# Performance work log

Measured on AMD Instinct MI355X. Metric: run time of the kernel, lower is better.

The kernel has to match this reference:

```python
import jax, jax.numpy as jnp
import numpy as np

B, L, HS = 2, 2048, 2048
NH, NKV, HD = 16, 4, 128
EPS = 1e-6
ROPE_BASE = 10000.0
SCALE = HD ** -0.5


def setup_inputs() -> dict:
    key = jax.random.key(0)
    ks = jax.random.split(key, 5)
    w = lambda k, shape: (jax.random.normal(k, shape, jnp.float32) * 0.02)
    return {
        "hidden_states": jax.random.normal(ks[0], (B, L, HS), jnp.float32),
        "Wq": w(ks[1], (HS, NH * HD)),
        "Wk": w(ks[2], (HS, NKV * HD)),
        "Wv": w(ks[3], (HS, NKV * HD)),
        "Wo": w(ks[4], (NH * HD, HS)),
        "q_norm_w": jnp.ones((HD,), jnp.float32),
        "k_norm_w": jnp.ones((HD,), jnp.float32),
    }


def _rmsnorm(x, w):
    return x * jax.lax.rsqrt(jnp.mean(x * x, axis=-1, keepdims=True) + EPS) * w


def _rope(x, cos, sin):
    # x: [B, L, heads, HD]; cos/sin: [1, L, 1, HD//2]
    x1, x2 = jnp.split(x, 2, axis=-1)
    return jnp.concatenate([x1 * cos - x2 * sin, x2 * cos + x1 * sin], axis=-1)


def reference(hidden_states, Wq, Wk, Wv, Wo, q_norm_w, k_norm_w):
    b, l, _ = hidden_states.shape
    n_rep = NH // NKV
    q = (hidden_states @ Wq).reshape(b, l, NH, HD)
    k = (hidden_states @ Wk).reshape(b, l, NKV, HD)
    v = (hidden_states @ Wv).reshape(b, l, NKV, HD)
    # QK RMSNorm over head_dim
    q = _rmsnorm(q, q_norm_w)
    k = _rmsnorm(k, k_norm_w)
    # RoPE with position_ids = arange(L)
    pos = jnp.arange(l, dtype=jnp.float32)
    inv_freq = 1.0 / (ROPE_BASE ** (jnp.arange(0, HD, 2, dtype=jnp.float32) / HD))
    ang = pos[:, None] * inv_freq  # [L, HD//2]
    cos = jnp.cos(ang)[None, :, None, :]
    sin = jnp.sin(ang)[None, :, None, :]
    q = _rope(q, cos, sin)
    k = _rope(k, cos, sin)
    # GQA: torch expand+reshape gives q head h -> kv head (h mod NKV);
    # reshape q to [B, L, n_rep, NKV, HD] (h = r*NKV + j) and contract per kv group.
    qg = q.reshape(b, l, n_rep, NKV, HD)
    scores = jnp.einsum("blrjd,bmjd->brjlm", qg, k) * SCALE  # [B, r, j, L, L]
    causal = jnp.tril(jnp.ones((l, l), dtype=bool))
    scores = jnp.where(causal, scores, -jnp.inf)
    probs = jax.nn.softmax(scores, axis=-1)
    out = jnp.einsum("brjlm,bmjd->blrjd", probs, v).reshape(b, l, NH * HD)
    return out @ Wo
```

## Files before the change

### kernel.cpp

```cpp
#include <hip/hip_runtime.h>
#include <hip/hip_bf16.h>

#define B_  2
#define L_  2048
#define HS_ 2048
#define NH_ 16
#define NKV_ 4
#define HD_ 128
#define EPS_ 1e-6f
#define SCALE_ 0.08838834764831843f
#define LOG2E_ 1.4426950408889634f

typedef __attribute__((ext_vector_type(8))) short bf16x8;
typedef __attribute__((ext_vector_type(4))) float f32x4;

__device__ __forceinline__ f32x4 mfma16(bf16x8 a, bf16x8 b, f32x4 c) {
    return __builtin_amdgcn_mfma_f32_16x16x32_bf16(a, b, c, 0, 0, 0);
}

__device__ __forceinline__ void async_copy16(void* lds, const void* g) {
    __builtin_amdgcn_global_load_lds(
        (const __attribute__((address_space(1))) unsigned int*)g,
        (__attribute__((address_space(3))) unsigned int*)lds,
        16, 0, 0);
}

__device__ __forceinline__ unsigned cvtpk(float lo, float hi) {
    unsigned r;
    asm("v_cvt_pk_bf16_f32 %0, %1, %2" : "=v"(r) : "v"(lo), "v"(hi));
    return r;
}

__global__ __launch_bounds__(256) void cvt_f32_bf16(const float* __restrict__ src,
                                                    __hip_bfloat16* __restrict__ dst,
                                                    int n4) {
    int i = blockIdx.x * 256 + threadIdx.x;
    if (i >= n4) return;
    float4 v = ((const float4*)src)[i];
    union { __hip_bfloat16 h[4]; short4 s; } u;
    u.h[0] = __float2bfloat16(v.x);
    u.h[1] = __float2bfloat16(v.y);
    u.h[2] = __float2bfloat16(v.z);
    u.h[3] = __float2bfloat16(v.w);
    ((short4*)dst)[i] = u.s;
}

__global__ __launch_bounds__(256) void transpose_cvt(const float* __restrict__ src,
                                                     __hip_bfloat16* __restrict__ dst,
                                                     int K, int N) {
    __shared__ float tile[32][33];
    int n0 = blockIdx.x * 32, k0 = blockIdx.y * 32;
    int tx = threadIdx.x & 31, ty = threadIdx.x >> 5;
#pragma unroll
    for (int i = 0; i < 32; i += 8)
        tile[ty + i][tx] = src[(size_t)(k0 + ty + i) * N + n0 + tx];
    __syncthreads();
#pragma unroll
    for (int i = 0; i < 32; i += 8)
        dst[(size_t)(n0 + ty + i) * K + k0 + tx] = __float2bfloat16(tile[tx][ty + i]);
}

__global__ __launch_bounds__(256) void v_transpose(const float* __restrict__ KV,
                                                   __hip_bfloat16* __restrict__ Vt) {
    __shared__ float tile[32][33];
    int bkv = blockIdx.z;
    int b = bkv >> 2, kv = bkv & 3;
    int l0 = blockIdx.x * 32, d0 = blockIdx.y * 32;
    int tx = threadIdx.x & 31, ty = threadIdx.x >> 5;
#pragma unroll
    for (int i = 0; i < 32; i += 8)
        tile[ty + i][tx] = KV[(size_t)(b * L_ + l0 + ty + i) * 1024 + 512 + kv * HD_ + d0 + tx];
    __syncthreads();
#pragma unroll
    for (int i = 0; i < 32; i += 8)
        Vt[((size_t)(b * NKV_ + kv) * HD_ + d0 + ty + i) * L_ + l0 + tx] =
            __float2bfloat16(tile[tx][ty + i]);
}

#define BM 128
#define BN 128
#define BKK 64
__global__ __launch_bounds__(256, 2) void gemm_bf16(const __hip_bfloat16* __restrict__ A,
                                                    const __hip_bfloat16* __restrict__ Bt,
                                                    float* __restrict__ C,
                                                    int M, int N, int K) {
    __shared__ __align__(16) __hip_bfloat16 sA[BM * BKK];
    __shared__ __align__(16) __hip_bfloat16 sB[BN * BKK];
    int t = threadIdx.x;
    int wave = t >> 6, lane = t & 63;
    int row16 = lane & 15, quad = lane >> 4;
    int m0 = blockIdx.x * BM, n0 = blockIdx.y * BN;
    int waveM = (wave >> 1) * 64, waveN = (wave & 1) * 64;
    f32x4 acc[4][4] = {};

    for (int k0 = 0; k0 < K; k0 += BKK) {
#pragma unroll
        for (int i = 0; i < 4; ++i) {
            int c = i * 256 + t;
            int r = c >> 3, kc = (c & 7) * 8;
            async_copy16(&sA[c * 8], A + (size_t)(m0 + r) * K + k0 + kc);
            async_copy16(&sB[c * 8], Bt + (size_t)(n0 + r) * K + k0 + kc);
        }
        __syncthreads();
#pragma unroll
        for (int kc = 0; kc < 2; ++kc) {
            bf16x8 a[4], b[4];
#pragma unroll
            for (int i = 0; i < 4; ++i)
                a[i] = *(const bf16x8*)&sA[(waveM + i * 16 + row16) * BKK + kc * 32 + quad * 8];
#pragma unroll
            for (int j = 0; j < 4; ++j)
                b[j] = *(const bf16x8*)&sB[(waveN + j * 16 + row16) * BKK + kc * 32 + quad * 8];
#pragma unroll
            for (int i = 0; i < 4; ++i)
#pragma unroll
                for (int j = 0; j < 4; ++j)
                    acc[i][j] = mfma16(a[i], b[j], acc[i][j]);
        }
        __syncthreads();
    }
#pragma unroll
    for (int i = 0; i < 4; ++i)
#pragma unroll
        for (int j = 0; j < 4; ++j) {
            int rbase = m0 + waveM + i * 16 + quad * 4;
            int col = n0 + waveN + j * 16 + row16;
#pragma unroll
            for (int r = 0; r < 4; ++r)
                C[(size_t)(rbase + r) * N + col] = acc[i][j][r];
        }
}

__global__ __launch_bounds__(256) void norm_rope(const float* __restrict__ X,
                                                 __hip_bfloat16* __restrict__ Y,
                                                 const float* __restrict__ w,
                                                 int log2nh, int in_stride, float oscale) {
    int row = blockIdx.x * 4 + (threadIdx.x >> 6);
    int lane = threadIdx.x & 63;
    int m = row >> log2nh;
    int head = row & ((1 << log2nh) - 1);
    int pos = m & (L_ - 1);
    const float* x = X + (size_t)m * in_stride + head * HD_;
    float x1 = x[lane], x2 = x[lane + 64];
    float ss = x1 * x1 + x2 * x2;
#pragma unroll
    for (int mm = 1; mm < 64; mm <<= 1) ss += __shfl_xor(ss, mm);
    float rms = rsqrtf(ss * (1.0f / 128.0f) + EPS_);
    float xn1 = x1 * rms * w[lane];
    float xn2 = x2 * rms * w[lane + 64];
    float inv_freq = __builtin_exp2f(-(float)lane * 0.20762050593046014f);
    float ang = (float)pos * inv_freq;
    float c = cosf(ang), s = sinf(ang);
    __hip_bfloat16* y = Y + (size_t)row * HD_;
    y[lane]      = __float2bfloat16((xn1 * c - xn2 * s) * oscale);
    y[lane + 64] = __float2bfloat16((xn2 * c + xn1 * s) * oscale);
}

__global__ __launch_bounds__(256, 2) void flash_attn(const __hip_bfloat16* __restrict__ Q,
                                                     const __hip_bfloat16* __restrict__ Kb,
                                                     const __hip_bfloat16* __restrict__ Vt,
                                                     __hip_bfloat16* __restrict__ O) {
    __shared__ __align__(16) __hip_bfloat16 sK[2][64 * 128];
    __shared__ __align__(16) __hip_bfloat16 sV[2][128 * 64];
    __shared__ __align__(16) __hip_bfloat16 sP[4][16 * 72];

    int t = threadIdx.x, wave = t >> 6, lane = t & 63;
    int row16 = lane & 15, quad = lane >> 4;
    int h = blockIdx.y, b = blockIdx.z;
    int kv = h & (NKV_ - 1);
    int x = blockIdx.x;
    int qtA = x, qtB = 31 - x;
    int nA = qtA + 1;
    const int nTot = 33;

    int e7 = row16 & 7;
    int kOff[4], vOff[2];
#pragma unroll
    for (int kc = 0; kc < 4; ++kc)
        kOff[kc] = row16 * 256 + (((kc * 4 + quad) ^ e7) * 16);
#pragma unroll
    for (int kc2 = 0; kc2 < 2; ++kc2)
        vOff[kc2] = row16 * 128 + (((kc2 * 4 + quad) ^ e7) * 16);

    const char* sKb = (const char*)&sK[0][0];
    const char* sVb = (const char*)&sV[0][0];
    char* myP = (char*)&sP[wave][0];
    int pW = row16 * 144 + quad * 8;
    int pR = row16 * 144 + quad * 16;

    const char* gK[4];
    const char* gV[4];
#pragma unroll
    for (int i = 0; i < 4; ++i) {
        int rk = wave * 16 + i * 4 + quad;
        int ck = row16 ^ (rk & 7);
        gK[i] = (const char*)(Kb + ((size_t)(b * L_ + rk) * NKV_ + kv) * HD_ + ck * 8);
        int rv = wave * 32 + i * 8 + (lane >> 3);
        int cv = (lane & 7) ^ (rv & 7);
        gV[i] = (const char*)(Vt + ((size_t)(b * NKV_ + kv) * HD_ + rv) * L_ + cv * 8);
    }
    char* dK = (char*)&sK[0][0] + wave * 4096 + lane * 16;
    char* dV = (char*)&sV[0][0] + wave * 4096 + lane * 16;

    bf16x8 qf[4];
    f32x4 accO[8];
    float lrow;
    int q0w = 0;

    auto loadQ = [&](int qt) {
        q0w = qt * 64 + wave * 16;
        const __hip_bfloat16* qbase =
            Q + ((size_t)(b * L_ + q0w + row16) * NH_ + h) * HD_ + quad * 8;
#pragma unroll
        for (int kc = 0; kc < 4; ++kc) qf[kc] = *(const bf16x8*)(qbase + kc * 32);
#pragma unroll
        for (int db = 0; db < 8; ++db) accO[db] = f32x4{0.f, 0.f, 0.f, 0.f};
        lrow = 0.f;
    };

    auto epilogue = [&]() {
        float l = lrow;
        l += __shfl_xor(l, 16);
        l += __shfl_xor(l, 32);
        float linv = 1.0f / l;
        __hip_bfloat16* obase = O + ((size_t)(b * L_ + q0w + row16) * NH_ + h) * HD_;
#pragma unroll
        for (int db = 0; db < 8; ++db) {
            union { __hip_bfloat16 h4[4]; short4 s4; } u;
#pragma unroll
            for (int r = 0; r < 4; ++r) u.h4[r] = __float2bfloat16(accO[db][r] * linv);
            *(short4*)(obase + db * 16 + quad * 4) = u.s4;
        }
    };

    auto stage = [&](int s1) {
        int kb64 = (s1 < nA ? s1 : s1 - nA) * 64;
        int buf = (s1 & 1) * 16384;
        int ko = kb64 * 1024;
        int vo = kb64 * 2;
#pragma unroll
        for (int i = 0; i < 4; ++i) {
            async_copy16(dK + buf + i * 1024, gK[i] + ko);
            async_copy16(dV + buf + i * 1024, gV[i] + vo);
        }
    };

    loadQ(qtA);
    stage(0);
    for (int s = 0; s < nTot; ++s) {
        __syncthreads();
        if (s + 1 < nTot) stage(s + 1);
        if (s == nA) { epilogue(); loadQ(qtB); }
        int kcur = (s < nA ? s : s - nA) * 64;
        const char* cK = sKb + (s & 1) * 16384;
        const char* cV = sVb + (s & 1) * 16384;

        f32x4 st[4];
        __builtin_amdgcn_s_setprio(1);
#pragma unroll
        for (int kb = 0; kb < 4; ++kb) {
            f32x4 acc = {};
#pragma unroll
            for (int kc = 0; kc < 4; ++kc) {
                bf16x8 kf = *(const bf16x8*)(cK + kb * 4096 + kOff[kc]);
                acc = mfma16(kf, qf[kc], acc);
            }
            st[kb] = acc;
        }
        __builtin_amdgcn_s_setprio(0);

        float p[4][4];
        if (kcur + 63 > q0w) {
            int qgRel = q0w + row16 - kcur - quad * 4;
#pragma unroll
            for (int kb = 0; kb < 4; ++kb)
#pragma unroll
                for (int r = 0; r < 4; ++r) {
                    float e = __builtin_exp2f(st[kb][r]);
                    p[kb][r] = (kb * 16 + r <= qgRel) ? e : 0.f;
                }
        } else {
#pragma unroll
            for (int kb = 0; kb < 4; ++kb)
#pragma unroll
                for (int r = 0; r < 4; ++r)
                    p[kb][r] = __builtin_exp2f(st[kb][r]);
        }
#pragma unroll
        for (int kb = 0; kb < 4; ++kb)
#pragma unroll
            for (int r = 0; r < 4; ++r) lrow += p[kb][r];

#pragma unroll
        for (int kb = 0; kb < 4; ++kb) {
            uint2 u;
            u.x = cvtpk(p[kb][0], p[kb][1]);
            u.y = cvtpk(p[kb][2], p[kb][3]);
            *(uint2*)(myP + pW + kb * 32) = u;
        }
        asm volatile("s_waitcnt lgkmcnt(0)" ::: "memory");
        bf16x8 pf[2];
        pf[0] = *(const bf16x8*)(myP + pR);
        pf[1] = *(const bf16x8*)(myP + pR + 64);

        __builtin_amdgcn_s_setprio(1);
#pragma unroll
        for (int db = 0; db < 8; ++db) {
#pragma unroll
            for (int kc2 = 0; kc2 < 2; ++kc2) {
                bf16x8 vf = *(const bf16x8*)(cV + db * 2048 + vOff[kc2]);
                accO[db] = mfma16(vf, pf[kc2], accO[db]);
            }
        }
        __builtin_amdgcn_s_setprio(0);
    }
    epilogue();
}

extern "C" void kernel_launch(void* const* d_in, const int* in_sizes, int n_in,
                              void* d_out, int out_size, void* d_ws, size_t ws_size,
                              hipStream_t stream) {
    const float* hidden = (const float*)d_in[0];
    const float* Wq = (const float*)d_in[1];
    const float* Wk = (const float*)d_in[2];
    const float* Wv = (const float*)d_in[3];
    const float* Wo = (const float*)d_in[4];
    const float* qw = (const float*)d_in[5];
    const float* kw = (const float*)d_in[6];
    float* out = (float*)d_out;

    char* ws = (char*)d_ws;
    size_t off = 0;
    auto alloc = [&](size_t bytes) { char* p = ws + off; off += (bytes + 255) & ~255ull; return p; };
    __hip_bfloat16* Wq_t = (__hip_bfloat16*)alloc((size_t)HS_ * NH_ * HD_ * 2);
    __hip_bfloat16* Wk_t = (__hip_bfloat16*)alloc((size_t)HS_ * NKV_ * HD_ * 2);
    __hip_bfloat16* Wv_t = (__hip_bfloat16*)alloc((size_t)HS_ * NKV_ * HD_ * 2);
    __hip_bfloat16* Wo_t = (__hip_bfloat16*)alloc((size_t)HS_ * NH_ * HD_ * 2);
    __hip_bfloat16* A_h  = (__hip_bfloat16*)alloc((size_t)B_ * L_ * HS_ * 2);
    float* kv_f32 = (float*)alloc((size_t)B_ * L_ * 1024 * 4);
    __hip_bfloat16* q_bf  = (__hip_bfloat16*)alloc((size_t)B_ * L_ * NH_ * HD_ * 2);
    __hip_bfloat16* k_bf  = (__hip_bfloat16*)alloc((size_t)B_ * L_ * NKV_ * HD_ * 2);
    __hip_bfloat16* vt_bf = (__hip_bfloat16*)alloc((size_t)B_ * NKV_ * HD_ * L_ * 2);
    float* q_f32 = out;
    __hip_bfloat16* attn_bf = A_h;

    const int M = B_ * L_;

    cvt_f32_bf16<<<(M * HS_ / 4 + 255) / 256, 256, 0, stream>>>(hidden, A_h, M * HS_ / 4);
    transpose_cvt<<<dim3(2048 / 32, 2048 / 32), 256, 0, stream>>>(Wq, Wq_t, HS_, 2048);
    transpose_cvt<<<dim3(512 / 32, 2048 / 32), 256, 0, stream>>>(Wk, Wk_t, HS_, 512);
    transpose_cvt<<<dim3(512 / 32, 2048 / 32), 256, 0, stream>>>(Wv, Wv_t, HS_, 512);
    transpose_cvt<<<dim3(2048 / 32, 2048 / 32), 256, 0, stream>>>(Wo, Wo_t, HS_, 2048);
    gemm_bf16<<<dim3(M / BM, 2048 / BN), 256, 0, stream>>>(A_h, Wq_t, q_f32, M, 2048, HS_);
    gemm_bf16<<<dim3(M / BM, 1024 / BN), 256, 0, stream>>>(A_h, Wk_t, kv_f32, M, 1024, HS_);
    norm_rope<<<(M * NH_) / 4, 256, 0, stream>>>(q_f32, q_bf, qw, 4, 2048, SCALE_ * LOG2E_);
    norm_rope<<<(M * NKV_) / 4, 256, 0, stream>>>(kv_f32, k_bf, kw, 2, 1024, 1.0f);
    v_transpose<<<dim3(L_ / 32, HD_ / 32, B_ * NKV_), 256, 0, stream>>>(kv_f32, vt_bf);
    flash_attn<<<dim3(16, NH_, B_), 256, 0, stream>>>(q_bf, k_bf, vt_bf, attn_bf);
    gemm_bf16<<<dim3(M / BM, 2048 / BN), 256, 0, stream>>>(attn_bf, Wo_t, out, M, 2048, HS_);
}
```

Baseline: 362.4 us.

## Fuse Q and KV projections into one 256x256-tile pipelined bf16 GEMM

Replaces the two separate Q and KV projection GEMMs with a single launch of a new 512-thread kernel. The new kernel uses 256x256 output tiles, double-buffered async global-to-LDS copies interleaved with MFMA phases, swizzled LDS addressing, an XCD-aware block remap and s_setprio around the MFMA blocks. Output columns are split between the Q buffer and the KV buffer. Bigger tiles raise arithmetic intensity and cut launches, but the kernel depends on Wq_t and Wk_t/Wv_t being contiguous (reading past Wq_t into the following allocations) and uses 128KB of LDS per block.

```diff
diff --git a/kernel.cpp b/kernel.cpp
--- a/kernel.cpp
+++ b/kernel.cpp
@@ -131,6 +131,177 @@
         }
 }
 
+#define GNT 32
+#define GKB 4096
+__global__ __launch_bounds__(512, 2) void gemm8_bf16(const __hip_bfloat16* __restrict__ A,
+                                                     const __hip_bfloat16* __restrict__ Bt,
+                                                     float* __restrict__ C1,
+                                                     float* __restrict__ C2,
+                                                     int Ntot, int splitN) {
+    __shared__ __align__(16) char lds[131072];
+    int t = threadIdx.x;
+    int w = t >> 6, lane = t & 63;
+    int row16 = lane & 15, quad = lane >> 4, e7 = row16 & 7;
+    int wr = w >> 2, wc = w & 3;
+
+    int gx = gridDim.x;
+    int nwg = gx * gridDim.y;
+    int bid = blockIdx.y * gx + blockIdx.x;
+    int cpx = nwg >> 3;
+    int swz = (bid & 7) * cpx + (bid >> 3);
+    int bx = swz % gx, by = swz / gx;
+    int m0 = bx * 256, n0 = by * 256;
+
+    const char* baseA[2];
+    const char* baseB[2];
+#pragma unroll
+    for (int kc = 0; kc < 2; ++kc) {
+        int so = ((kc * 4 + quad) ^ e7) << 4;
+        baseA[kc] = lds + wr * 16384 + row16 * 128 + so;
+        baseB[kc] = lds + 65536 + wc * 8192 + row16 * 128 + so;
+    }
+
+    int r8 = lane >> 3;
+    int sl = (lane & 7) ^ r8;
+    char* dstA = lds + wr * 16384 + (w & 3) * 2048 + lane * 16;
+    char* dstB = lds + 65536 + (w >> 1) * 8192 + (w & 1) * 2048 + lane * 16;
+    const char* gA = (const char*)A +
+        (size_t)(m0 + wr * 128 + (w & 3) * 16 + r8) * GKB + sl * 16;
+    const char* gB = (const char*)Bt +
+        (size_t)(n0 + (w >> 1) * 64 + (w & 1) * 16 + r8) * GKB + sl * 16;
+
+    f32x4 acc[8][4] = {};
+    bf16x8 a[4][2], b[2][2];
+
+#pragma unroll
+    for (int i = 0; i < 2; ++i) async_copy16(dstA + i * 1024, gA + i * 32768);
+#pragma unroll
+    for (int i = 0; i < 2; ++i) async_copy16(dstB + i * 1024, gB + i * 32768);
+#pragma unroll
+    for (int i = 0; i < 2; ++i) async_copy16(dstB + 4096 + i * 1024, gB + 131072 + i * 32768);
+#pragma unroll
+    for (int i = 0; i < 2; ++i) async_copy16(dstA + 8192 + i * 1024, gA + 262144 + i * 32768);
+
+    for (int Tb = 0; Tb < GNT; Tb += 2) {
+#pragma unroll
+        for (int u = 0; u < 2; ++u) {
+            const int T = Tb + u;
+            const int cu = u * 32768, du = (u ^ 1) * 32768;
+            const int tn = (T + 1 < GNT ? T + 1 : T) * 128;
+
+            asm volatile("s_waitcnt vmcnt(4)" ::: "memory");
+            __builtin_amdgcn_s_barrier();
+            __builtin_amdgcn_sched_barrier(0);
+#pragma unroll
+            for (int mi = 0; mi < 4; ++mi)
+#pragma unroll
+                for (int kc = 0; kc < 2; ++kc)
+                    a[mi][kc] = *(const bf16x8*)(baseA[kc] + cu + mi * 2048);
+#pragma unroll
+            for (int ni = 0; ni < 2; ++ni)
+#pragma unroll
+                for (int kc = 0; kc < 2; ++kc)
+                    b[ni][kc] = *(const bf16x8*)(baseB[kc] + cu + ni * 2048);
+#pragma unroll
+            for (int i = 0; i < 2; ++i)
+                async_copy16(dstA + du + i * 1024, gA + tn + i * 32768);
+            asm volatile("s_waitcnt lgkmcnt(0)" ::: "memory");
+            __builtin_amdgcn_sched_barrier(0);
+            __builtin_amdgcn_s_setprio(1);
+#pragma unroll
+            for (int mi = 0; mi < 4; ++mi)
+#pragma unroll
+                for (int ni = 0; ni < 2; ++ni)
+#pragma unroll
+                    for (int kc = 0; kc < 2; ++kc)
+                        acc[mi][ni] = mfma16(a[mi][kc], b[ni][kc], acc[mi][ni]);
+            __builtin_amdgcn_s_setprio(0);
+
+            asm volatile("s_waitcnt vmcnt(4)" ::: "memory");
+            __builtin_amdgcn_s_barrier();
+            __builtin_amdgcn_sched_barrier(0);
+#pragma unroll
+            for (int ni = 0; ni < 2; ++ni)
+#pragma unroll
+                for (int kc = 0; kc < 2; ++kc)
+                    b[ni][kc] = *(const bf16x8*)(baseB[kc] + cu + 4096 + ni * 2048);
+#pragma unroll
+            for (int i = 0; i < 2; ++i)
+                async_copy16(dstB + du + i * 1024, gB + tn + i * 32768);
+            asm volatile("s_waitcnt lgkmcnt(0)" ::: "memory");
+            __builtin_amdgcn_sched_barrier(0);
+            __builtin_amdgcn_s_setprio(1);
+#pragma unroll
+            for (int mi = 0; mi < 4; ++mi)
+#pragma unroll
+                for (int ni = 0; ni < 2; ++ni)
+#pragma unroll
+                    for (int kc = 0; kc < 2; ++kc)
+                        acc[mi][2 + ni] = mfma16(a[mi][kc], b[ni][kc], acc[mi][2 + ni]);
+            __builtin_amdgcn_s_setprio(0);
+
+            asm volatile("s_waitcnt vmcnt(4)" ::: "memory");
+            __builtin_amdgcn_s_barrier();
+            __builtin_amdgcn_sched_barrier(0);
+#pragma unroll
+            for (int mi = 0; mi < 4; ++mi)
+#pragma unroll
+                for (int kc = 0; kc < 2; ++kc)
+                    a[mi][kc] = *(const bf16x8*)(baseA[kc] + cu + 8192 + mi * 2048);
+#pragma unroll
+            for (int i = 0; i < 2; ++i)
+                async_copy16(dstB + du + 4096 + i * 1024, gB + 131072 + tn + i * 32768);
+            asm volatile("s_waitcnt lgkmcnt(0)" ::: "memory");
+            __builtin_amdgcn_sched_barrier(0);
+            __builtin_amdgcn_s_setprio(1);
+#pragma unroll
+            for (int mi = 0; mi < 4; ++mi)
+#pragma unroll
+                for (int ni = 0; ni < 2; ++ni)
+#pragma unroll
+                    for (int kc = 0; kc < 2; ++kc)
+                        acc[4 + mi][2 + ni] = mfma16(a[mi][kc], b[ni][kc], acc[4 + mi][2 + ni]);
+            __builtin_amdgcn_s_setprio(0);
+
+            __builtin_amdgcn_s_barrier();
+            __builtin_amdgcn_sched_barrier(0);
+#pragma unroll
+            for (int ni = 0; ni < 2; ++ni)
+#pragma unroll
+                for (int kc = 0; kc < 2; ++kc)
+                    b[ni][kc] = *(const bf16x8*)(baseB[kc] + cu + ni * 2048);
+#pragma unroll
+            for (int i = 0; i < 2; ++i)
+                async_copy16(dstA + du + 8192 + i * 1024, gA + 262144 + tn + i * 32768);
+            asm volatile("s_waitcnt lgkmcnt(0)" ::: "memory");
+            __builtin_amdgcn_sched_barrier(0);
+            __builtin_amdgcn_s_setprio(1);
+#pragma unroll
+            for (int mi = 0; mi < 4; ++mi)
+#pragma unroll
+                for (int ni = 0; ni < 2; ++ni)
+#pragma unroll
+                    for (int kc = 0; kc < 2; ++kc)
+                        acc[4 + mi][ni] = mfma16(a[mi][kc], b[ni][kc], acc[4 + mi][ni]);
+            __builtin_amdgcn_s_setprio(0);
+        }
+    }
+
+    float* Cb; int cs, ccol0;
+    if (n0 < splitN) { Cb = C1; cs = splitN; ccol0 = n0; }
+    else             { Cb = C2; cs = Ntot - splitN; ccol0 = n0 - splitN; }
+#pragma unroll
+    for (int mi = 0; mi < 8; ++mi)
+#pragma unroll
+        for (int ni = 0; ni < 4; ++ni) {
+            int rbase = m0 + wr * 128 + mi * 16 + quad * 4;
+            int col = ccol0 + wc * 64 + ni * 16 + row16;
+#pragma unroll
+            for (int r = 0; r < 4; ++r)
+                Cb[(size_t)(rbase + r) * cs + col] = acc[mi][ni][r];
+        }
+}
+
 __global__ __launch_bounds__(256) void norm_rope(const float* __restrict__ X,
                                                  __hip_bfloat16* __restrict__ Y,
                                                  const float* __restrict__ w,
@@ -351,8 +522,8 @@
     transpose_cvt<<<dim3(512 / 32, 2048 / 32), 256, 0, stream>>>(Wk, Wk_t, HS_, 512);
     transpose_cvt<<<dim3(512 / 32, 2048 / 32), 256, 0, stream>>>(Wv, Wv_t, HS_, 512);
     transpose_cvt<<<dim3(2048 / 32, 2048 / 32), 256, 0, stream>>>(Wo, Wo_t, HS_, 2048);
-    gemm_bf16<<<dim3(M / BM, 2048 / BN), 256, 0, stream>>>(A_h, Wq_t, q_f32, M, 2048, HS_);
-    gemm_bf16<<<dim3(M / BM, 1024 / BN), 256, 0, stream>>>(A_h, Wk_t, kv_f32, M, 1024, HS_);
+    gemm8_bf16<<<dim3(M / 256, 3072 / 256), 512, 0, stream>>>(
+        A_h, Wq_t, q_f32, kv_f32, 3072, 2048);
     norm_rope<<<(M * NH_) / 4, 256, 0, stream>>>(q_f32, q_bf, qw, 4, 2048, SCALE_ * LOG2E_);
     norm_rope<<<(M * NKV_) / 4, 256, 0, stream>>>(kv_f32, k_bf, kw, 2, 1024, 1.0f);
     v_transpose<<<dim3(L_ / 32, HD_ / 32, B_ * NKV_), 256, 0, stream>>>(kv_f32, vt_bf);
```

After: 318.7 us. -12.1%, faster.

## Double-buffer GEMMs, fuse QKV projection, and merge prep and norm kernels

Applied to the files above, without the earlier changes.

Replaces the single-buffered GEMM with a double-buffered one. It uses XOR-swizzled LDS layout, explicit waitcnt and barrier scheduling, s_setprio around MFMA blocks, and block-index swizzling across XCDs. The Q and KV projections become one GEMM with N=3072, relying on the transposed Wq, Wk and Wv buffers being contiguous in the workspace. The bf16 conversion and weight transposes are merged into one launch, and so are the Q/K norm-rope and V-transpose kernels. These changes target load latency, LDS bank conflicts and launch overhead. In exchange the GEMM is hardcoded for K=2048 and depends on the workspace layout.

```diff
diff --git a/kernel.cpp b/kernel.cpp
--- a/kernel.cpp
+++ b/kernel.cpp
@@ -31,25 +31,32 @@
     return r;
 }
 
-__global__ __launch_bounds__(256) void cvt_f32_bf16(const float* __restrict__ src,
-                                                    __hip_bfloat16* __restrict__ dst,
-                                                    int n4) {
-    int i = blockIdx.x * 256 + threadIdx.x;
-    if (i >= n4) return;
-    float4 v = ((const float4*)src)[i];
-    union { __hip_bfloat16 h[4]; short4 s; } u;
-    u.h[0] = __float2bfloat16(v.x);
-    u.h[1] = __float2bfloat16(v.y);
-    u.h[2] = __float2bfloat16(v.z);
-    u.h[3] = __float2bfloat16(v.w);
-    ((short4*)dst)[i] = u.s;
-}
-
-__global__ __launch_bounds__(256) void transpose_cvt(const float* __restrict__ src,
-                                                     __hip_bfloat16* __restrict__ dst,
-                                                     int K, int N) {
+__global__ __launch_bounds__(256) void fused_prep(
+    const float* __restrict__ hidden, __hip_bfloat16* __restrict__ A_h,
+    const float* __restrict__ Wq, __hip_bfloat16* __restrict__ Wq_t,
+    const float* __restrict__ Wk, __hip_bfloat16* __restrict__ Wk_t,
+    const float* __restrict__ Wv, __hip_bfloat16* __restrict__ Wv_t,
+    const float* __restrict__ Wo, __hip_bfloat16* __restrict__ Wo_t) {
     __shared__ float tile[32][33];
-    int n0 = blockIdx.x * 32, k0 = blockIdx.y * 32;
+    int bid = blockIdx.x;
+    if (bid < 8192) {
+        int i = bid * 256 + threadIdx.x;
+        float4 v = ((const float4*)hidden)[i];
+        union { __hip_bfloat16 h[4]; short4 s; } u;
+        u.h[0] = __float2bfloat16(v.x);
+        u.h[1] = __float2bfloat16(v.y);
+        u.h[2] = __float2bfloat16(v.z);
+        u.h[3] = __float2bfloat16(v.w);
+        ((short4*)A_h)[i] = u.s;
+        return;
+    }
+    const float* src; __hip_bfloat16* dst; int N, tb;
+    if (bid < 12288)      { tb = bid - 8192;  src = Wq; dst = Wq_t; N = 2048; }
+    else if (bid < 13312) { tb = bid - 12288; src = Wk; dst = Wk_t; N = 512;  }
+    else if (bid < 14336) { tb = bid - 13312; src = Wv; dst = Wv_t; N = 512;  }
+    else                  { tb = bid - 14336; src = Wo; dst = Wo_t; N = 2048; }
+    int nt = N >> 5;
+    int n0 = (tb % nt) * 32, k0 = (tb / nt) * 32;
     int tx = threadIdx.x & 31, ty = threadIdx.x >> 5;
 #pragma unroll
     for (int i = 0; i < 32; i += 8)
@@ -57,86 +64,14 @@
     __syncthreads();
 #pragma unroll
     for (int i = 0; i < 32; i += 8)
-        dst[(size_t)(n0 + ty + i) * K + k0 + tx] = __float2bfloat16(tile[tx][ty + i]);
-}
-
-__global__ __launch_bounds__(256) void v_transpose(const float* __restrict__ KV,
-                                                   __hip_bfloat16* __restrict__ Vt) {
-    __shared__ float tile[32][33];
-    int bkv = blockIdx.z;
-    int b = bkv >> 2, kv = bkv & 3;
-    int l0 = blockIdx.x * 32, d0 = blockIdx.y * 32;
-    int tx = threadIdx.x & 31, ty = threadIdx.x >> 5;
-#pragma unroll
-    for (int i = 0; i < 32; i += 8)
-        tile[ty + i][tx] = KV[(size_t)(b * L_ + l0 + ty + i) * 1024 + 512 + kv * HD_ + d0 + tx];
-    __syncthreads();
-#pragma unroll
-    for (int i = 0; i < 32; i += 8)
-        Vt[((size_t)(b * NKV_ + kv) * HD_ + d0 + ty + i) * L_ + l0 + tx] =
-            __float2bfloat16(tile[tx][ty + i]);
-}
-
-#define BM 128
-#define BN 128
-#define BKK 64
-__global__ __launch_bounds__(256, 2) void gemm_bf16(const __hip_bfloat16* __restrict__ A,
-                                                    const __hip_bfloat16* __restrict__ Bt,
-                                                    float* __restrict__ C,
-                                                    int M, int N, int K) {
-    __shared__ __align__(16) __hip_bfloat16 sA[BM * BKK];
-    __shared__ __align__(16) __hip_bfloat16 sB[BN * BKK];
-    int t = threadIdx.x;
-    int wave = t >> 6, lane = t & 63;
-    int row16 = lane & 15, quad = lane >> 4;
-    int m0 = blockIdx.x * BM, n0 = blockIdx.y * BN;
-    int waveM = (wave >> 1) * 64, waveN = (wave & 1) * 64;
-    f32x4 acc[4][4] = {};
-
-    for (int k0 = 0; k0 < K; k0 += BKK) {
-#pragma unroll
-        for (int i = 0; i < 4; ++i) {
-            int c = i * 256 + t;
-            int r = c >> 3, kc = (c & 7) * 8;
-            async_copy16(&sA[c * 8], A + (size_t)(m0 + r) * K + k0 + kc);
-            async_copy16(&sB[c * 8], Bt + (size_t)(n0 + r) * K + k0 + kc);
-        }
-        __syncthreads();
-#pragma unroll
-        for (int kc = 0; kc < 2; ++kc) {
-            bf16x8 a[4], b[4];
-#pragma unroll
-            for (int i = 0; i < 4; ++i)
-                a[i] = *(const bf16x8*)&sA[(waveM + i * 16 + row16) * BKK + kc * 32 + quad * 8];
-#pragma unroll
-            for (int j = 0; j < 4; ++j)
-                b[j] = *(const bf16x8*)&sB[(waveN + j * 16 + row16) * BKK + kc * 32 + quad * 8];
-#pragma unroll
-            for (int i = 0; i < 4; ++i)
-#pragma unroll
-                for (int j = 0; j < 4; ++j)
-                    acc[i][j] = mfma16(a[i], b[j], acc[i][j]);
-        }
-        __syncthreads();
-    }
-#pragma unroll
-    for (int i = 0; i < 4; ++i)
-#pragma unroll
-        for (int j = 0; j < 4; ++j) {
-            int rbase = m0 + waveM + i * 16 + quad * 4;
-            int col = n0 + waveN + j * 16 + row16;
-#pragma unroll
-            for (int r = 0; r < 4; ++r)
-                C[(size_t)(rbase + r) * N + col] = acc[i][j][r];
-        }
-}
-
-__global__ __launch_bounds__(256) void norm_rope(const float* __restrict__ X,
-                                                 __hip_bfloat16* __restrict__ Y,
-                                                 const float* __restrict__ w,
-                                                 int log2nh, int in_stride, float oscale) {
-    int row = blockIdx.x * 4 + (threadIdx.x >> 6);
-    int lane = threadIdx.x & 63;
+        dst[(size_t)(n0 + ty + i) * HS_ + k0 + tx] = __float2bfloat16(tile[tx][ty + i]);
+}
+
+__device__ __forceinline__ void norm_rope_row(const float* __restrict__ X,
+                                              __hip_bfloat16* __restrict__ Y,
+                                              const float* __restrict__ w,
+                                              int row, int lane,
+                                              int log2nh, int in_stride, float oscale) {
     int m = row >> log2nh;
     int head = row & ((1 << log2nh) - 1);
     int pos = m & (L_ - 1);
@@ -154,6 +89,171 @@
     __hip_bfloat16* y = Y + (size_t)row * HD_;
     y[lane]      = __float2bfloat16((xn1 * c - xn2 * s) * oscale);
     y[lane + 64] = __float2bfloat16((xn2 * c + xn1 * s) * oscale);
+}
+
+__global__ __launch_bounds__(256) void fused_norm_v(
+    const float* __restrict__ q_f32, __hip_bfloat16* __restrict__ q_bf,
+    const float* __restrict__ kv_f32, __hip_bfloat16* __restrict__ k_bf,
+    __hip_bfloat16* __restrict__ vt_bf,
+    const float* __restrict__ qw, const float* __restrict__ kw) {
+    __shared__ float tile[32][33];
+    int bid = blockIdx.x;
+    int lane = threadIdx.x & 63;
+    if (bid < 16384) {
+        int row = bid * 4 + (threadIdx.x >> 6);
+        norm_rope_row(q_f32, q_bf, qw, row, lane, 4, 2048, SCALE_ * LOG2E_);
+        return;
+    }
+    if (bid < 20480) {
+        int row = (bid - 16384) * 4 + (threadIdx.x >> 6);
+        norm_rope_row(kv_f32, k_bf, kw, row, lane, 2, 1024, 1.0f);
+        return;
+    }
+    int vbid = bid - 20480;
+    int xb = vbid & 63, yb = (vbid >> 6) & 3, zb = vbid >> 8;
+    int b = zb >> 2, kv = zb & 3;
+    int l0 = xb * 32, d0 = yb * 32;
+    int tx = threadIdx.x & 31, ty = threadIdx.x >> 5;
+#pragma unroll
+    for (int i = 0; i < 32; i += 8)
+        tile[ty + i][tx] = kv_f32[(size_t)(b * L_ + l0 + ty + i) * 1024 + 512 + kv * HD_ + d0 + tx];
+    __syncthreads();
+#pragma unroll
+    for (int i = 0; i < 32; i += 8)
+        vt_bf[((size_t)(b * NKV_ + kv) * HD_ + d0 + ty + i) * L_ + l0 + tx] =
+            __float2bfloat16(tile[tx][ty + i]);
+}
+
+#define GNT 32
+#define GKB 4096
+template<int BN, bool SPLIT>
+__global__ __launch_bounds__(256, 2) void gemm_db(const __hip_bfloat16* __restrict__ A,
+                                                  const __hip_bfloat16* __restrict__ Bt,
+                                                  float* __restrict__ C1,
+                                                  float* __restrict__ C2) {
+    constexpr int NB = BN / 32;
+    constexpr int NI = BN / 32;
+    constexpr int BUFA = 16384;
+    constexpr int BUFB = BN * 128;
+    __shared__ __align__(16) char lds[2 * BUFA + 2 * BUFB];
+    int t = threadIdx.x;
+    int w = t >> 6, lane = t & 63;
+    int row16 = lane & 15, quad = lane >> 4, e7 = row16 & 7;
+    int wr = w >> 1, wc = w & 1;
+
+    int gx = gridDim.x;
+    int nwg = gx * gridDim.y;
+    int bid = blockIdx.y * gx + blockIdx.x;
+    int cpx = nwg >> 3;
+    int swz = (bid & 7) * cpx + (bid >> 3);
+    int bx = swz % gx, by = swz / gx;
+    int m0 = bx * 128, n0 = by * BN;
+
+    const char* baseA[2];
+    const char* baseB[2];
+#pragma unroll
+    for (int kc = 0; kc < 2; ++kc) {
+        int so = ((kc * 4 + quad) ^ e7) << 4;
+        baseA[kc] = lds + (wr * 64 + row16) * 128 + so;
+        baseB[kc] = lds + 2 * BUFA + (wc * (BN / 2) + row16) * 128 + so;
+    }
+
+    int r8 = t >> 3;
+    int sl = (t & 7) ^ (r8 & 7);
+    char* dA = lds + r8 * 128 + (t & 7) * 16;
+    char* dB = lds + 2 * BUFA + r8 * 128 + (t & 7) * 16;
+    const char* gA = (const char*)A + (size_t)(m0 + r8) * GKB + sl * 16;
+    const char* gB = (const char*)Bt + (size_t)(n0 + r8) * GKB + sl * 16;
+    const int arow[4] = {0, 64, 32, 96};
+
+    f32x4 acc[4][NI] = {};
+    bf16x8 a[2][2], b[NI][2];
+
+#pragma unroll
+    for (int j = 0; j < NB; ++j) async_copy16(dB + j * 4096, gB + (size_t)j * 32 * GKB);
+#pragma unroll
+    for (int i = 0; i < 4; ++i) async_copy16(dA + arow[i] * 128, gA + (size_t)arow[i] * GKB);
+
+    for (int T = 0; T < GNT; ++T) {
+        const int cuA = (T & 1) * BUFA, duA = ((T + 1) & 1) * BUFA;
+        const int cuB = (T & 1) * BUFB, duB = ((T + 1) & 1) * BUFB;
+        const int tn = (T + 1 < GNT ? T + 1 : T) * 128;
+
+        asm volatile("s_waitcnt vmcnt(2)" ::: "memory");
+        __builtin_amdgcn_s_barrier();
+        __builtin_amdgcn_sched_barrier(0);
+#pragma unroll
+        for (int mi = 0; mi < 2; ++mi)
+#pragma unroll
+            for (int kc = 0; kc < 2; ++kc)
+                a[mi][kc] = *(const bf16x8*)(baseA[kc] + cuA + mi * 2048);
+#pragma unroll
+        for (int ni = 0; ni < NI; ++ni)
+#pragma unroll
+            for (int kc = 0; kc < 2; ++kc)
+                b[ni][kc] = *(const bf16x8*)(baseB[kc] + cuB + ni * 2048);
+#pragma unroll
+        for (int j = 0; j < NB; ++j)
+            async_copy16(dB + duB + j * 4096, gB + (size_t)j * 32 * GKB + tn);
+        asm volatile("s_waitcnt lgkmcnt(0)" ::: "memory");
+        __builtin_amdgcn_sched_barrier(0);
+        __builtin_amdgcn_s_setprio(1);
+#pragma unroll
+        for (int mi = 0; mi < 2; ++mi)
+#pragma unroll
+            for (int ni = 0; ni < NI; ++ni)
+#pragma unroll
+                for (int kc = 0; kc < 2; ++kc)
+                    acc[mi][ni] = mfma16(a[mi][kc], b[ni][kc], acc[mi][ni]);
+        __builtin_amdgcn_s_setprio(0);
+
+        asm volatile("s_waitcnt vmcnt(%0)" :: "i"(NB) : "memory");
+        __builtin_amdgcn_s_barrier();
+        __builtin_amdgcn_sched_barrier(0);
+#pragma unroll
+        for (int mi = 0; mi < 2; ++mi)
+#pragma unroll
+            for (int kc = 0; kc < 2; ++kc)
+                a[mi][kc] = *(const bf16x8*)(baseA[kc] + cuA + 4096 + mi * 2048);
+#pragma unroll
+        for (int i = 0; i < 4; ++i)
+            async_copy16(dA + duA + arow[i] * 128, gA + (size_t)arow[i] * GKB + tn);
+        asm volatile("s_waitcnt lgkmcnt(0)" ::: "memory");
+        __builtin_amdgcn_sched_barrier(0);
+        __builtin_amdgcn_s_setprio(1);
+#pragma unroll
+        for (int mi = 0; mi < 2; ++mi)
+#pragma unroll
+            for (int ni = 0; ni < NI; ++ni)
+#pragma unroll
+                for (int kc = 0; kc < 2; ++kc)
+                    acc[2 + mi][ni] = mfma16(a[mi][kc], b[ni][kc], acc[2 + mi][ni]);
+        __builtin_amdgcn_s_setprio(0);
+    }
+    asm volatile("s_waitcnt vmcnt(0)" ::: "memory");
+
+#pragma unroll
+    for (int mi = 0; mi < 4; ++mi)
+#pragma unroll
+        for (int ni = 0; ni < NI; ++ni) {
+            int rbase = m0 + wr * 64 + mi * 16 + quad * 4;
+            int col = n0 + wc * (BN / 2) + ni * 16 + row16;
+            if (SPLIT) {
+                if (col < 2048) {
+#pragma unroll
+                    for (int r = 0; r < 4; ++r)
+                        C1[(size_t)(rbase + r) * 2048 + col] = acc[mi][ni][r];
+                } else {
+#pragma unroll
+                    for (int r = 0; r < 4; ++r)
+                        C2[(size_t)(rbase + r) * 1024 + (col - 2048)] = acc[mi][ni][r];
+                }
+            } else {
+#pragma unroll
+                for (int r = 0; r < 4; ++r)
+                    C1[(size_t)(rbase + r) * 2048 + col] = acc[mi][ni][r];
+            }
+        }
 }
 
 __global__ __launch_bounds__(256, 2) void flash_attn(const __hip_bfloat16* __restrict__ Q,
@@ -346,16 +446,11 @@
 
     const int M = B_ * L_;
 
-    cvt_f32_bf16<<<(M * HS_ / 4 + 255) / 256, 256, 0, stream>>>(hidden, A_h, M * HS_ / 4);
-    transpose_cvt<<<dim3(2048 / 32, 2048 / 32), 256, 0, stream>>>(Wq, Wq_t, HS_, 2048);
-    transpose_cvt<<<dim3(512 / 32, 2048 / 32), 256, 0, stream>>>(Wk, Wk_t, HS_, 512);
-    transpose_cvt<<<dim3(512 / 32, 2048 / 32), 256, 0, stream>>>(Wv, Wv_t, HS_, 512);
-    transpose_cvt<<<dim3(2048 / 32, 2048 / 32), 256, 0, stream>>>(Wo, Wo_t, HS_, 2048);
-    gemm_bf16<<<dim3(M / BM, 2048 / BN), 256, 0, stream>>>(A_h, Wq_t, q_f32, M, 2048, HS_);
-    gemm_bf16<<<dim3(M / BM, 1024 / BN), 256, 0, stream>>>(A_h, Wk_t, kv_f32, M, 1024, HS_);
-    norm_rope<<<(M * NH_) / 4, 256, 0, stream>>>(q_f32, q_bf, qw, 4, 2048, SCALE_ * LOG2E_);
-    norm_rope<<<(M * NKV_) / 4, 256, 0, stream>>>(kv_f32, k_bf, kw, 2, 1024, 1.0f);
-    v_transpose<<<dim3(L_ / 32, HD_ / 32, B_ * NKV_), 256, 0, stream>>>(kv_f32, vt_bf);
+    fused_prep<<<18432, 256, 0, stream>>>(hidden, A_h, Wq, Wq_t, Wk, Wk_t, Wv, Wv_t, Wo, Wo_t);
+    gemm_db<192, true><<<dim3(M / 128, 3072 / 192), 256, 0, stream>>>(
+        A_h, Wq_t, q_f32, kv_f32);
+    fused_norm_v<<<22528, 256, 0, stream>>>(q_f32, q_bf, kv_f32, k_bf, vt_bf, qw, kw);
     flash_attn<<<dim3(16, NH_, B_), 256, 0, stream>>>(q_bf, k_bf, vt_bf, attn_bf);
-    gemm_bf16<<<dim3(M / BM, 2048 / BN), 256, 0, stream>>>(attn_bf, Wo_t, out, M, 2048, HS_);
-}
+    gemm_db<128, false><<<dim3(M / 128, 2048 / 128), 256, 0, stream>>>(
+        attn_bf, Wo_t, out, nullptr);
+}
```

Result: faster. 295.8 us (-18.4%).
